# Kernel optimization log

Hardware: AMD Instinct MI355X
Metric: run time of the kernel (lower is better)

## Reference

```python
import jax, jax.numpy as jnp
import numpy as np

N = 2048          # n_nodes
H = 8             # nheads
ALPHA = 0.2       # leaky-relu slope
NEG = -9e15       # mask value used by pyGAT
# (in_dim, per-head hidden, out_dim) for the six GAT blocks of GMHAAE(256, ...)
DIMS = [(256, 128, 128), (128, 256, 256), (256, 512, 384),
        (384, 512, 256), (256, 256, 128), (128, 128, 256)]


def setup_inputs() -> dict:
    key = jax.random.key(0)
    ks = jax.random.split(key, 64)
    inp = {}
    inp["x"] = jax.random.normal(ks[0], (N, 256), dtype=jnp.float32)
    a = (jax.random.uniform(ks[1], (N, N)) < 0.01).astype(jnp.float32)
    adj = jnp.clip(jnp.maximum(a, a.T) + jnp.eye(N, dtype=jnp.float32), 0.0, 1.0)
    inp["adj"] = adj
    ki = 2
    for i, (fin, hid, fout) in enumerate(DIMS, start=1):
        s1 = (2.0 / (fin + hid)) ** 0.5
        inp[f"p{i}_Wh"] = jax.random.normal(ks[ki], (H, fin, hid), dtype=jnp.float32) * s1; ki += 1
        inp[f"p{i}_ah"] = jax.random.normal(ks[ki], (H, 2 * hid), dtype=jnp.float32) * 0.1; ki += 1
        s2 = (2.0 / (H * hid + fout)) ** 0.5
        inp[f"p{i}_Wo"] = jax.random.normal(ks[ki], (H * hid, fout), dtype=jnp.float32) * s2; ki += 1
        inp[f"p{i}_ao"] = jax.random.normal(ks[ki], (2 * fout,), dtype=jnp.float32) * 0.1; ki += 1
    return inp


def _gat_block(x, adj, Wh, ah, Wo, ao):
    """pyGAT GAT block: H concat heads (elu) -> single out head -> elu. Eval mode (no dropout)."""
    n = x.shape[0]
    D = Wh.shape[2]
    h = jnp.einsum('nf,hfd->hnd', x, Wh)                       # [H,N,D]
    s1 = jnp.einsum('hnd,hd->hn', h, ah[:, :D])                # a^T [Wh_i]
    s2 = jnp.einsum('hnd,hd->hn', h, ah[:, D:])                # a^T [Wh_j]
    e = jax.nn.leaky_relu(s1[:, :, None] + s2[:, None, :], ALPHA)   # [H,N,N]
    att = jax.nn.softmax(jnp.where(adj[None] > 0, e, NEG), axis=-1)
    hcat = jax.nn.elu(jnp.einsum('hnm,hmd->hnd', att, h))      # concat=True -> elu per head
    hcat = hcat.transpose(1, 0, 2).reshape(n, -1)              # [N, H*D]
    # output attention head (concat=False)
    D2 = Wo.shape[1]
    ho = hcat @ Wo                                             # [N,D2]
    eo = jax.nn.leaky_relu((ho @ ao[:D2])[:, None] + (ho @ ao[D2:])[None, :], ALPHA)
    ato = jax.nn.softmax(jnp.where(adj > 0, eo, NEG), axis=-1)
    return jax.nn.elu(ato @ ho)                                # F.elu in GAT.forward


def reference(x, adj,
              p1_Wh, p1_ah, p1_Wo, p1_ao,
              p2_Wh, p2_ah, p2_Wo, p2_ao,
              p3_Wh, p3_ah, p3_Wo, p3_ao,
              p4_Wh, p4_ah, p4_Wo, p4_ao,
              p5_Wh, p5_ah, p5_Wo, p5_ao,
              p6_Wh, p6_ah, p6_Wo, p6_ao):
    layers = [(p1_Wh, p1_ah, p1_Wo, p1_ao), (p2_Wh, p2_ah, p2_Wo, p2_ao),
              (p3_Wh, p3_ah, p3_Wo, p3_ao), (p4_Wh, p4_ah, p4_Wo, p4_ao),
              (p5_Wh, p5_ah, p5_Wo, p5_ao), (p6_Wh, p6_ah, p6_Wo, p6_ao)]
    h = x
    for (Wh, ah, Wo, ao) in layers:   # fixed 6-layer encoder-decoder stack
        h = _gat_block(h, adj, Wh, ah, Wo, ao)
    return h
```

## Files before the change

kernel.cpp:

```cpp
#include <hip/hip_runtime.h>
#include <hip/hip_bf16.h>
#include <math.h>

#define NN 2048
#define NH 8
#define LRALPHA 0.2f

typedef short bf16x8 __attribute__((ext_vector_type(8)));
typedef float f32x4  __attribute__((ext_vector_type(4)));

static __device__ __forceinline__ float lrelu(float x){ return x > 0.f ? x : LRALPHA * x; }
static __device__ __forceinline__ float elu(float x){ return x > 0.f ? x : expm1f(x); }

static __device__ __forceinline__ unsigned short f2bf(float v){
    unsigned u = __float_as_uint(v);
    unsigned r = (u + 0x7fffu + ((u >> 16) & 1u)) >> 16;
    return (unsigned short)r;
}
static __device__ __forceinline__ float bf2f(unsigned short b){
    return __uint_as_float(((unsigned)b) << 16);
}
static __device__ __forceinline__ float blo(unsigned u){ return __uint_as_float(u << 16); }
static __device__ __forceinline__ float bhi(unsigned u){ return __uint_as_float(u & 0xffff0000u); }

static __device__ __forceinline__ void gload16(const void* g, void* l){
    __builtin_amdgcn_global_load_lds((const __attribute__((address_space(1))) void*)g,
                                     (__attribute__((address_space(3))) void*)l, 16, 0, 0);
}

__global__ void k_count(const float* __restrict__ adj, int* __restrict__ deg) {
    int gw   = (blockIdx.x * blockDim.x + threadIdx.x) >> 6;
    int lane = threadIdx.x & 63;
    if (gw >= NN) return;
    const float* row = adj + (size_t)gw * NN;
    int cnt = 0;
    for (int j = lane; j < NN; j += 64) cnt += (row[j] > 0.f) ? 1 : 0;
    #pragma unroll
    for (int off = 32; off; off >>= 1) cnt += __shfl_down(cnt, off);
    if (lane == 0) deg[gw] = cnt;
}

__global__ void k_scan(const int* __restrict__ deg, int* __restrict__ rp) {
    __shared__ int a[NN], b[NN];
    int t = threadIdx.x;
    for (int i = t; i < NN; i += 1024) a[i] = deg[i];
    __syncthreads();
    int* src = a; int* dst = b;
    for (int off = 1; off < NN; off <<= 1) {
        for (int i = t; i < NN; i += 1024)
            dst[i] = src[i] + (i >= off ? src[i - off] : 0);
        __syncthreads();
        int* tmp = src; src = dst; dst = tmp;
    }
    for (int i = t; i < NN; i += 1024) rp[i + 1] = src[i];
    if (t == 0) rp[0] = 0;
}

__global__ void k_fill(const float* __restrict__ adj, const int* __restrict__ rp,
                       int* __restrict__ ci) {
    int gw   = (blockIdx.x * blockDim.x + threadIdx.x) >> 6;
    int lane = threadIdx.x & 63;
    if (gw >= NN) return;
    const float* row = adj + (size_t)gw * NN;
    int base = rp[gw];
    for (int j0 = 0; j0 < NN; j0 += 64) {
        bool v = row[j0 + lane] > 0.f;
        unsigned long long m = __ballot(v);
        int pos = __popcll(m & ((1ULL << lane) - 1ULL));
        if (v) ci[base + pos] = j0 + lane;
        base += __popcll(m);
    }
}

__global__ void k_split(const float* __restrict__ src, unsigned short* __restrict__ hi,
                        unsigned short* __restrict__ lo, int n4) {
    int i = blockIdx.x * 256 + threadIdx.x;
    if (i >= n4) return;
    float4 v = ((const float4*)src)[i];
    ushort4 h, l;
    h.x = f2bf(v.x); l.x = f2bf(v.x - bf2f(h.x));
    h.y = f2bf(v.y); l.y = f2bf(v.y - bf2f(h.y));
    h.z = f2bf(v.z); l.z = f2bf(v.z - bf2f(h.z));
    h.w = f2bf(v.w); l.w = f2bf(v.w - bf2f(h.w));
    ((ushort4*)hi)[i] = h;
    ((ushort4*)lo)[i] = l;
}

struct TSDesc {
    const float* B[12];
    unsigned short* bh[12];
    unsigned short* bl[12];
    int K[12], Nc[12], hs[12];
    int start[13];
};

__global__ __launch_bounds__(256) void k_tsplit_all(TSDesc d) {
    __shared__ float t[64][65];
    int b = blockIdx.x;
    int s = 0;
    while (b >= d.start[s + 1]) s++;
    int lb = b - d.start[s];
    int K = d.K[s], Nc = d.Nc[s], hs = d.hs[s];
    int tilesX = K >> 6;
    int kb = (lb % tilesX) * 64, cb = (lb / tilesX) * 64;
    const float* B = d.B[s];
    unsigned short* bth = d.bh[s];
    unsigned short* btl = d.bl[s];

    int tid = threadIdx.x;
    #pragma unroll
    for (int i = 0; i < 16; i++) {
        int idx = i * 256 + tid;
        int kk = idx >> 6, cc = idx & 63;
        int c = cb + cc, k = kb + kk;
        float v;
        if (hs < 0) v = B[(size_t)k * Nc + c];
        else {
            int hid = 1 << hs; int head = c >> hs; int dd = c & (hid - 1);
            v = B[((size_t)head * K + k) * hid + dd];
        }
        t[kk][cc] = v;
    }
    __syncthreads();
    #pragma unroll
    for (int i = 0; i < 16; i++) {
        int idx = i * 256 + tid;
        int cc = idx >> 6, kk = idx & 63;
        float v = t[kk][cc];
        unsigned short h = f2bf(v);
        size_t o = (size_t)(cb + cc) * K + kb + kk;
        bth[o] = h;
        btl[o] = f2bf(v - bf2f(h));
    }
}

template<int OUT, int NT>
__global__ __launch_bounds__(256) void k_mfma(
    const unsigned short* __restrict__ Ah, const unsigned short* __restrict__ Al,
    const unsigned short* __restrict__ Bh, const unsigned short* __restrict__ Bl,
    float* __restrict__ Cf, unsigned short* __restrict__ Cb, int Nc, int K, int Kc,
    const float* __restrict__ avec, float* __restrict__ sg1, float* __restrict__ sg2,
    int hs, int aoff, int nx, int nz, int zcol)
{
    constexpr int ALB = 4096;
    constexpr int BHB = (NT == 3) ? 8192 : 4096;
    constexpr int BLB = BHB + 2048;
    __shared__ unsigned short lds[(NT == 3) ? 12288 : 8192];
    int tid = threadIdx.x, lane = tid & 63, w = tid >> 6;

    int g = blockIdx.x;
    int xcd = g & 7, q = g >> 3;
    int x, y, z;
    if (zcol) {
        int zper = nz >> 3;
        z = xcd + 8 * (q % zper);
        int r = q / zper;
        int nxy = nx * 16;
        int r2 = r + xcd * (nxy >> 3); if (r2 >= nxy) r2 -= nxy;
        x = r2 % nx; y = r2 / nx;
    } else {
        y = xcd + 8 * (q & 1);
        x = q >> 1; z = 0;
    }
    int m0 = y * 128, n0 = x * 64;
    int kbeg = z * Kc;

    int ra0 = tid >> 2;       int ga0 = ((tid & 3) - (ra0 >> 1)) & 3;
    int ra1 = 64 + (tid >> 2); int ga1 = ((tid & 3) - (ra1 >> 1)) & 3;
    int rb  = tid >> 2;       int gb  = ((tid & 3) - (rb >> 1)) & 3;
    const unsigned short* pAh0 = Ah + (size_t)(m0 + ra0) * K + kbeg + ga0 * 8;
    const unsigned short* pAh1 = Ah + (size_t)(m0 + ra1) * K + kbeg + ga1 * 8;
    const unsigned short* pAl0 = (NT == 3) ? Al + (size_t)(m0 + ra0) * K + kbeg + ga0 * 8 : nullptr;
    const unsigned short* pAl1 = (NT == 3) ? Al + (size_t)(m0 + ra1) * K + kbeg + ga1 * 8 : nullptr;
    const unsigned short* pBh  = Bh + (size_t)(n0 + rb) * K + kbeg + gb * 8;
    const unsigned short* pBl  = Bl + (size_t)(n0 + rb) * K + kbeg + gb * 8;
    unsigned short* dA0 = &lds[w * 512];
    unsigned short* dA1 = &lds[2048 + w * 512];
    unsigned short* dB  = &lds[BHB + w * 512];

    int wr = w >> 1, wc = w & 1;
    int offA[4], offB[2];
    #pragma unroll
    for (int m = 0; m < 4; m++) {
        int row = wr * 64 + m * 16 + (lane & 15); int gg = lane >> 4;
        offA[m] = (row * 4 + ((gg + (row >> 1)) & 3)) * 8;
    }
    #pragma unroll
    for (int n = 0; n < 2; n++) {
        int row = wc * 32 + n * 16 + (lane & 15); int gg = lane >> 4;
        offB[n] = (row * 4 + ((gg + (row >> 1)) & 3)) * 8;
    }

    f32x4 acc[4][2];
    #pragma unroll
    for (int m = 0; m < 4; m++)
        #pragma unroll
        for (int n = 0; n < 2; n++) acc[m][n] = (f32x4){0.f, 0.f, 0.f, 0.f};

    int nk = Kc >> 5;
    for (int ks = 0; ks < nk; ks++) {
        gload16(pAh0, dA0);
        gload16(pAh1, dA1);
        if (NT == 3) { gload16(pAl0, dA0 + ALB); gload16(pAl1, dA1 + ALB); }
        gload16(pBh, dB);
        gload16(pBl, dB + 2048);
        pAh0 += 32; pAh1 += 32;
        if (NT == 3) { pAl0 += 32; pAl1 += 32; }
        pBh += 32; pBl += 32;
        __syncthreads();
        bf16x8 ah[4], al[4], bh[2], bl[2];
        #pragma unroll
        for (int m = 0; m < 4; m++) {
            ah[m] = *(const bf16x8*)&lds[offA[m]];
            if (NT == 3) al[m] = *(const bf16x8*)&lds[ALB + offA[m]];
        }
        #pragma unroll
        for (int n = 0; n < 2; n++) {
            bh[n] = *(const bf16x8*)&lds[BHB + offB[n]];
            bl[n] = *(const bf16x8*)&lds[BLB + offB[n]];
        }
        #pragma unroll
        for (int m = 0; m < 4; m++)
            #pragma unroll
            for (int n = 0; n < 2; n++) {
                acc[m][n] = __builtin_amdgcn_mfma_f32_16x16x32_bf16(ah[m], bh[n], acc[m][n], 0, 0, 0);
                if (NT == 3)
                    acc[m][n] = __builtin_amdgcn_mfma_f32_16x16x32_bf16(al[m], bh[n], acc[m][n], 0, 0, 0);
                acc[m][n] = __builtin_amdgcn_mfma_f32_16x16x32_bf16(ah[m], bl[n], acc[m][n], 0, 0, 0);
            }
        __syncthreads();
    }

    #pragma unroll
    for (int m = 0; m < 4; m++)
        #pragma unroll
        for (int n = 0; n < 2; n++) {
            int row = m0 + wr * 64 + m * 16 + (lane >> 4) * 4;
            int col = n0 + wc * 32 + n * 16 + (lane & 15);
            #pragma unroll
            for (int r = 0; r < 4; r++) {
                float v = acc[m][n][r];
                if (OUT == 0) Cb[(size_t)(row + r) * Nc + col] = f2bf(v);
                else          atomicAdd(&Cf[(size_t)(row + r) * Nc + col], v);
            }
        }

    int head = (hs >= 0) ? (n0 >> hs) : 0;
    const float* ab = avec + head * 2 * aoff;
    float av1[2], av2[2];
    int colbase = n0 + wc * 32 + (lane & 15);
    #pragma unroll
    for (int n = 0; n < 2; n++) {
        int c = colbase + n * 16;
        int dd = (hs >= 0) ? (c & (aoff - 1)) : c;
        av1[n] = ab[dd];
        av2[n] = ab[dd + aoff];
    }
    #pragma unroll
    for (int m = 0; m < 4; m++)
        #pragma unroll
        for (int r = 0; r < 4; r++) {
            float p1 = 0.f, p2 = 0.f;
            #pragma unroll
            for (int n = 0; n < 2; n++) {
                float v = acc[m][n][r];
                p1 += v * av1[n];
                p2 += v * av2[n];
            }
            #pragma unroll
            for (int o = 1; o < 16; o <<= 1) {
                p1 += __shfl_xor(p1, o);
                p2 += __shfl_xor(p2, o);
            }
            if ((lane & 15) == 0) {
                int row = m0 + wr * 64 + m * 16 + (lane >> 4) * 4 + r;
                atomicAdd(&sg1[head * NN + row], p1);
                atomicAdd(&sg2[head * NN + row], p2);
            }
        }
}

__global__ __launch_bounds__(64) void k_aggb(
    const unsigned short* __restrict__ hh, const float* __restrict__ s1,
    const float* __restrict__ s2, const int* __restrict__ rp, const int* __restrict__ ci,
    unsigned short* __restrict__ outH, int hid, int HD, int c8sh)
{
    __shared__ float    wls[64];
    __shared__ unsigned cls[64];

    int blk  = blockIdx.x;
    int head = blk & (NH - 1);
    int i    = blk >> 3;
    int lane = threadIdx.x;
    int base = rp[i], deg = rp[i + 1] - base;
    float s1i = s1[head * NN + i];
    const float* s2h = s2 + head * NN;

    int C8  = 1 << c8sh;
    int G   = 64 >> c8sh;
    int col = lane & (C8 - 1);
    int grp = lane >> c8sh;

    const uint4* h4 = (const uint4*)hh;
    unsigned hoff8 = (unsigned)(head * hid) >> 3;
    unsigned ld8   = (unsigned)HD >> 3;

    float m_run = -1e30f, s_run = 0.f;
    float a0=0,a1=0,a2=0,a3=0,a4=0,a5=0,a6=0,a7=0;

    for (int k0 = 0; k0 < deg; k0 += 64) {
        int n = min(64, deg - k0);
        float e = -1e30f;
        unsigned coff = 0;
        if (lane < n) {
            int j = ci[base + k0 + lane];
            e = lrelu(s1i + s2h[j]);
            coff = (unsigned)j * ld8 + hoff8;
        }
        float bm = e;
        #pragma unroll
        for (int o = 32; o; o >>= 1) bm = fmaxf(bm, __shfl_xor(bm, o));
        float m2 = fmaxf(m_run, bm);
        float wv = (lane < n) ? expf(e - m2) : 0.f;
        float bs = wv;
        #pragma unroll
        for (int o = 32; o; o >>= 1) bs += __shfl_xor(bs, o);
        float scale = expf(m_run - m2);
        s_run = s_run * scale + bs;
        a0*=scale; a1*=scale; a2*=scale; a3*=scale;
        a4*=scale; a5*=scale; a6*=scale; a7*=scale;
        m_run = m2;
        wls[lane] = wv;
        cls[lane] = coff;

        float q0=0,q1=0,q2=0,q3=0,q4=0,q5=0,q6=0,q7=0;
        int k = grp;
        for (; k + G < n; k += 2 * G) {
            float w0 = wls[k], w1 = wls[k + G];
            uint4 u0 = h4[cls[k]     + col];
            uint4 u1 = h4[cls[k + G] + col];
            a0 += w0 * blo(u0.x); a1 += w0 * bhi(u0.x);
            a2 += w0 * blo(u0.y); a3 += w0 * bhi(u0.y);
            a4 += w0 * blo(u0.z); a5 += w0 * bhi(u0.z);
            a6 += w0 * blo(u0.w); a7 += w0 * bhi(u0.w);
            q0 += w1 * blo(u1.x); q1 += w1 * bhi(u1.x);
            q2 += w1 * blo(u1.y); q3 += w1 * bhi(u1.y);
            q4 += w1 * blo(u1.z); q5 += w1 * bhi(u1.z);
            q6 += w1 * blo(u1.w); q7 += w1 * bhi(u1.w);
        }
        if (k < n) {
            float w0 = wls[k];
            uint4 u0 = h4[cls[k] + col];
            a0 += w0 * blo(u0.x); a1 += w0 * bhi(u0.x);
            a2 += w0 * blo(u0.y); a3 += w0 * bhi(u0.y);
            a4 += w0 * blo(u0.z); a5 += w0 * bhi(u0.z);
            a6 += w0 * blo(u0.w); a7 += w0 * bhi(u0.w);
        }
        a0+=q0; a1+=q1; a2+=q2; a3+=q3; a4+=q4; a5+=q5; a6+=q6; a7+=q7;
    }

    #pragma unroll
    for (int o = 64; o > 1; o >>= 1) {
        if (o > C8) {
            int m = o >> 1;
            a0 += __shfl_xor(a0, m); a1 += __shfl_xor(a1, m);
            a2 += __shfl_xor(a2, m); a3 += __shfl_xor(a3, m);
            a4 += __shfl_xor(a4, m); a5 += __shfl_xor(a5, m);
            a6 += __shfl_xor(a6, m); a7 += __shfl_xor(a7, m);
        }
    }

    if (grp == 0) {
        float inv = 1.f / s_run;
        float v[8] = {a0*inv,a1*inv,a2*inv,a3*inv,a4*inv,a5*inv,a6*inv,a7*inv};
        #pragma unroll
        for (int e2 = 0; e2 < 8; e2++) v[e2] = elu(v[e2]);
        unsigned short hh_[8];
        #pragma unroll
        for (int e2 = 0; e2 < 8; e2++) hh_[e2] = f2bf(v[e2]);
        size_t ob = ((size_t)i * HD + head * hid) >> 3;
        uint4 ph;
        ph.x = (unsigned)hh_[0] | ((unsigned)hh_[1] << 16);
        ph.y = (unsigned)hh_[2] | ((unsigned)hh_[3] << 16);
        ph.z = (unsigned)hh_[4] | ((unsigned)hh_[5] << 16);
        ph.w = (unsigned)hh_[6] | ((unsigned)hh_[7] << 16);
        ((uint4*)outH)[ob + col] = ph;
    }
}

__global__ __launch_bounds__(64) void k_aggs(
    const float* __restrict__ hsrc, const float* __restrict__ t1, const float* __restrict__ t2,
    const int* __restrict__ rp, const int* __restrict__ ci,
    float* __restrict__ outF, unsigned short* __restrict__ outH,
    int fout, int SCtot)
{
    __shared__ float    wls[64];
    __shared__ unsigned cls[64];

    int blk = blockIdx.x;
    int i   = blk / SCtot;
    int sc  = blk - i * SCtot;
    int lane = threadIdx.x;
    int base = rp[i], deg = rp[i + 1] - base;
    float s1i = t1[i];

    int C4tot = fout >> 2;
    int soff  = sc * 64;
    int C4s   = min(64, C4tot - soff);
    int c4sh  = 31 - __clz(C4s);
    int col = lane & (C4s - 1);
    int grp = lane >> c4sh;
    int G   = 64 >> c4sh;

    const float4* h4 = (const float4*)hsrc;
    unsigned ld4 = (unsigned)fout >> 2;

    float m_run = -1e30f, s_run = 0.f;
    float4 acc = make_float4(0.f, 0.f, 0.f, 0.f);

    for (int k0 = 0; k0 < deg; k0 += 64) {
        int n = min(64, deg - k0);
        float e = -1e30f;
        unsigned coff = 0;
        if (lane < n) {
            int j = ci[base + k0 + lane];
            e = lrelu(s1i + t2[j]);
            coff = (unsigned)j * ld4 + soff;
        }
        float bm = e;
        #pragma unroll
        for (int o = 32; o; o >>= 1) bm = fmaxf(bm, __shfl_xor(bm, o));
        float m2 = fmaxf(m_run, bm);
        float wv = (lane < n) ? expf(e - m2) : 0.f;
        float bs = wv;
        #pragma unroll
        for (int o = 32; o; o >>= 1) bs += __shfl_xor(bs, o);
        float scale = expf(m_run - m2);
        s_run = s_run * scale + bs;
        acc.x *= scale; acc.y *= scale; acc.z *= scale; acc.w *= scale;
        m_run = m2;
        wls[lane] = wv;
        cls[lane] = coff;

        float4 q = make_float4(0,0,0,0);
        int k = grp;
        for (; k + G < n; k += 2 * G) {
            float w0 = wls[k], w1 = wls[k + G];
            float4 h0 = h4[cls[k]     + col];
            float4 h1 = h4[cls[k + G] + col];
            acc.x += w0 * h0.x; acc.y += w0 * h0.y; acc.z += w0 * h0.z; acc.w += w0 * h0.w;
            q.x   += w1 * h1.x; q.y   += w1 * h1.y; q.z   += w1 * h1.z; q.w   += w1 * h1.w;
        }
        if (k < n) {
            float w0 = wls[k];
            float4 h0 = h4[cls[k] + col];
            acc.x += w0 * h0.x; acc.y += w0 * h0.y; acc.z += w0 * h0.z; acc.w += w0 * h0.w;
        }
        acc.x += q.x; acc.y += q.y; acc.z += q.z; acc.w += q.w;
    }

    #pragma unroll
    for (int o = 64; o > 1; o >>= 1) {
        if (o > C4s) {
            int m = o >> 1;
            acc.x += __shfl_xor(acc.x, m); acc.y += __shfl_xor(acc.y, m);
            acc.z += __shfl_xor(acc.z, m); acc.w += __shfl_xor(acc.w, m);
        }
    }

    if (grp == 0) {
        float inv = 1.f / s_run;
        float4 val;
        val.x = elu(acc.x * inv); val.y = elu(acc.y * inv);
        val.z = elu(acc.z * inv); val.w = elu(acc.w * inv);
        size_t o4 = (size_t)i * ld4 + soff + col;
        if (outF) ((float4*)outF)[o4] = val;
        ushort4 h;
        h.x = f2bf(val.x); h.y = f2bf(val.y);
        h.z = f2bf(val.z); h.w = f2bf(val.w);
        ((ushort4*)outH)[o4] = h;
    }
}

extern "C" void kernel_launch(void* const* d_in, const int* in_sizes, int n_in,
                              void* d_out, int out_size, void* d_ws, size_t ws_size,
                              hipStream_t stream)
{
    const float* x   = (const float*)d_in[0];
    const float* adj = (const float*)d_in[1];
    struct L { int fin, hid, fout; };
    const L dims[6] = {{256,128,128},{128,256,256},{256,512,384},
                       {384,512,256},{256,256,128},{128,128,256}};
    const int SKwo[6] = {16, 8, 8, 8, 16, 8};
    const int SB = 2 * NH * NN + 2 * NN;

    char* ws = (char*)d_ws;
    size_t off = 0;
    auto alloc = [&](size_t bytes) -> void* {
        void* p = ws + off;
        off = (off + bytes + 255) & ~(size_t)255;
        return p;
    };
    int*   rp   = (int*)alloc((NN + 1) * sizeof(int));
    int*   deg  = (int*)alloc(NN * sizeof(int));
    int*   ci   = (int*)alloc((size_t)(1 << 20) * sizeof(int));
    unsigned short* hh  = (unsigned short*)alloc((size_t)NN * 4096 * 2);
    unsigned short* ghi = (unsigned short*)alloc((size_t)NN * 4096 * 2);
    unsigned short* xhi = (unsigned short*)alloc((size_t)NN * 512 * 2);
    unsigned short* xlo = (unsigned short*)alloc((size_t)NN * 512 * 2);
    float* sball  = (float*)alloc((size_t)6 * SB * sizeof(float));
    float* hoball = (float*)alloc((size_t)NN * 1408 * sizeof(float));

    int hoboff[6]; { int acc = 0; for (int l = 0; l < 6; l++) { hoboff[l] = acc; acc += dims[l].fout; } }

    unsigned short* whh[6]; unsigned short* whl[6];
    unsigned short* woh[6]; unsigned short* wol[6];
    TSDesc td;
    int nblk = 0;
    for (int l = 0; l < 6; l++) {
        int fin = dims[l].fin, hid = dims[l].hid, fout = dims[l].fout;
        int HD = NH * hid;
        size_t szWh = (size_t)fin * HD, szWo = (size_t)HD * fout;
        whh[l] = (unsigned short*)alloc(szWh * 2);
        whl[l] = (unsigned short*)alloc(szWh * 2);
        woh[l] = (unsigned short*)alloc(szWo * 2);
        wol[l] = (unsigned short*)alloc(szWo * 2);
        int hs = (hid == 128) ? 7 : (hid == 256) ? 8 : 9;
        td.B[2*l] = (const float*)d_in[2 + l * 4 + 0];
        td.bh[2*l] = whh[l]; td.bl[2*l] = whl[l];
        td.K[2*l] = fin; td.Nc[2*l] = HD; td.hs[2*l] = hs;
        td.start[2*l] = nblk; nblk += (fin / 64) * (HD / 64);
        td.B[2*l+1] = (const float*)d_in[2 + l * 4 + 2];
        td.bh[2*l+1] = woh[l]; td.bl[2*l+1] = wol[l];
        td.K[2*l+1] = HD; td.Nc[2*l+1] = fout; td.hs[2*l+1] = -1;
        td.start[2*l+1] = nblk; nblk += (HD / 64) * (fout / 64);
    }
    td.start[12] = nblk;

    hipMemsetAsync(sball, 0, (size_t)6 * SB * sizeof(float), stream);
    hipMemsetAsync(hoball, 0, (size_t)NN * 1408 * sizeof(float), stream);
    k_count<<<NN / 4, 256, 0, stream>>>(adj, deg);
    k_scan <<<1, 1024, 0, stream>>>(deg, rp);
    k_fill <<<NN / 4, 256, 0, stream>>>(adj, rp, ci);
    k_split<<<(NN * 256 / 4 + 255) / 256, 256, 0, stream>>>(x, xhi, xlo, NN * 256 / 4);
    k_tsplit_all<<<nblk, 256, 0, stream>>>(td);

    for (int l = 0; l < 6; l++) {
        int fin = dims[l].fin, hid = dims[l].hid, fout = dims[l].fout;
        int HD = NH * hid;
        int hs = (hid == 128) ? 7 : (hid == 256) ? 8 : 9;
        int c8sh = hs - 3;
        const float* ah = (const float*)d_in[2 + l * 4 + 1];
        const float* ao = (const float*)d_in[2 + l * 4 + 3];

        float* s1 = sball + (size_t)l * SB;
        float* s2 = s1 + NH * NN;
        float* t1 = s2 + NH * NN;
        float* t2 = t1 + NN;
        float* hob = hoball + (size_t)NN * hoboff[l];

        int nx1 = HD / 64;
        if (l == 0)
            k_mfma<0,3><<<nx1 * 16, 256, 0, stream>>>(xhi, xlo, whh[l], whl[l], nullptr, hh, HD,
                                                      fin, fin, ah, s1, s2, hs, hid, nx1, 1, 0);
        else
            k_mfma<0,2><<<nx1 * 16, 256, 0, stream>>>(xhi, nullptr, whh[l], whl[l], nullptr, hh, HD,
                                                      fin, fin, ah, s1, s2, hs, hid, nx1, 1, 0);

        k_aggb<<<NN * NH, 64, 0, stream>>>(hh, s1, s2, rp, ci, ghi, hid, HD, c8sh);

        int sko = SKwo[l];
        int nx2 = fout / 64;
        k_mfma<1,2><<<nx2 * 16 * sko, 256, 0, stream>>>(ghi, nullptr, woh[l], wol[l], hob, nullptr,
                                                        fout, HD, HD / sko, ao, t1, t2, -1, fout,
                                                        nx2, sko, 1);

        float* outF = (l == 5) ? (float*)d_out : nullptr;
        int SCtot = (fout / 4 + 63) / 64;
        k_aggs<<<NN * SCtot, 64, 0, stream>>>(hob, t1, t2, rp, ci, outF, xhi, fout, SCtot);
    }
}
```

Measured before the change: 534.0 us.

## Replace split-K atomic accumulation with partial buffers and a reduction kernel

The split-K output-projection GEMM now stores each K-slice's fp32 tile in its own slice of a partial buffer instead of atomically adding into a zeroed accumulator, and it no longer computes the attention score dots itself. A new per-row kernel sums the slices, writes the projected features and computes the two output-attention score vectors in one pass. This drops the large memset and the global float atomics for the feature tile and the score vectors, and makes the result deterministic. In exchange it writes and re-reads several full copies of the output, up to 16 for some layers, and adds one kernel launch per layer.

```diff
diff --git a/kernel.cpp b/kernel.cpp
--- a/kernel.cpp
+++ b/kernel.cpp
@@ -231,6 +231,7 @@
         __syncthreads();
     }
 
+    size_t pbase = (size_t)z * NN * Nc;
     #pragma unroll
     for (int m = 0; m < 4; m++)
         #pragma unroll
@@ -241,43 +242,75 @@
             for (int r = 0; r < 4; r++) {
                 float v = acc[m][n][r];
                 if (OUT == 0) Cb[(size_t)(row + r) * Nc + col] = f2bf(v);
-                else          atomicAdd(&Cf[(size_t)(row + r) * Nc + col], v);
+                else          Cf[pbase + (size_t)(row + r) * Nc + col] = v;
             }
         }
 
-    int head = (hs >= 0) ? (n0 >> hs) : 0;
-    const float* ab = avec + head * 2 * aoff;
-    float av1[2], av2[2];
-    int colbase = n0 + wc * 32 + (lane & 15);
-    #pragma unroll
-    for (int n = 0; n < 2; n++) {
-        int c = colbase + n * 16;
-        int dd = (hs >= 0) ? (c & (aoff - 1)) : c;
-        av1[n] = ab[dd];
-        av2[n] = ab[dd + aoff];
-    }
-    #pragma unroll
-    for (int m = 0; m < 4; m++)
-        #pragma unroll
-        for (int r = 0; r < 4; r++) {
-            float p1 = 0.f, p2 = 0.f;
+    if (OUT == 0) {
+        int head = (hs >= 0) ? (n0 >> hs) : 0;
+        const float* ab = avec + head * 2 * aoff;
+        float av1[2], av2[2];
+        int colbase = n0 + wc * 32 + (lane & 15);
+        #pragma unroll
+        for (int n = 0; n < 2; n++) {
+            int c = colbase + n * 16;
+            int dd = (hs >= 0) ? (c & (aoff - 1)) : c;
+            av1[n] = ab[dd];
+            av2[n] = ab[dd + aoff];
+        }
+        #pragma unroll
+        for (int m = 0; m < 4; m++)
             #pragma unroll
-            for (int n = 0; n < 2; n++) {
-                float v = acc[m][n][r];
-                p1 += v * av1[n];
-                p2 += v * av2[n];
+            for (int r = 0; r < 4; r++) {
+                float p1 = 0.f, p2 = 0.f;
+                #pragma unroll
+                for (int n = 0; n < 2; n++) {
+                    float v = acc[m][n][r];
+                    p1 += v * av1[n];
+                    p2 += v * av2[n];
+                }
+                #pragma unroll
+                for (int o = 1; o < 16; o <<= 1) {
+                    p1 += __shfl_xor(p1, o);
+                    p2 += __shfl_xor(p2, o);
+                }
+                if ((lane & 15) == 0) {
+                    int row = m0 + wr * 64 + m * 16 + (lane >> 4) * 4 + r;
+                    atomicAdd(&sg1[head * NN + row], p1);
+                    atomicAdd(&sg2[head * NN + row], p2);
+                }
             }
-            #pragma unroll
-            for (int o = 1; o < 16; o <<= 1) {
-                p1 += __shfl_xor(p1, o);
-                p2 += __shfl_xor(p2, o);
-            }
-            if ((lane & 15) == 0) {
-                int row = m0 + wr * 64 + m * 16 + (lane >> 4) * 4 + r;
-                atomicAdd(&sg1[head * NN + row], p1);
-                atomicAdd(&sg2[head * NN + row], p2);
-            }
-        }
+    }
+}
+
+__global__ __launch_bounds__(64) void k_red(
+    const float* __restrict__ part, float* __restrict__ ho,
+    const float* __restrict__ ao, float* __restrict__ t1, float* __restrict__ t2,
+    int fout, int sko)
+{
+    int row = blockIdx.x;
+    int lane = threadIdx.x;
+    int C4 = fout >> 2;
+    const float4* p4 = (const float4*)part;
+    size_t stride4 = (size_t)NN * C4;
+    float d1 = 0.f, d2 = 0.f;
+    for (int c = lane; c < C4; c += 64) {
+        size_t o = (size_t)row * C4 + c;
+        float4 s = p4[o];
+        for (int zz = 1; zz < sko; zz++) {
+            float4 v = p4[o + (size_t)zz * stride4];
+            s.x += v.x; s.y += v.y; s.z += v.z; s.w += v.w;
+        }
+        ((float4*)ho)[o] = s;
+        int cc = c * 4;
+        d1 += s.x * ao[cc]        + s.y * ao[cc + 1]
+            + s.z * ao[cc + 2]    + s.w * ao[cc + 3];
+        d2 += s.x * ao[fout + cc]     + s.y * ao[fout + cc + 1]
+            + s.z * ao[fout + cc + 2] + s.w * ao[fout + cc + 3];
+    }
+    #pragma unroll
+    for (int o = 32; o; o >>= 1) { d1 += __shfl_xor(d1, o); d2 += __shfl_xor(d2, o); }
+    if (lane == 0) { t1[row] = d1; t2[row] = d2; }
 }
 
 __global__ __launch_bounds__(64) void k_aggb(
@@ -492,7 +525,7 @@
     const L dims[6] = {{256,128,128},{128,256,256},{256,512,384},
                        {384,512,256},{256,256,128},{128,128,256}};
     const int SKwo[6] = {16, 8, 8, 8, 16, 8};
-    const int SB = 2 * NH * NN + 2 * NN;
+    const int SB = 2 * NH * NN;
 
     char* ws = (char*)d_ws;
     size_t off = 0;
@@ -509,9 +542,9 @@
     unsigned short* xhi = (unsigned short*)alloc((size_t)NN * 512 * 2);
     unsigned short* xlo = (unsigned short*)alloc((size_t)NN * 512 * 2);
     float* sball  = (float*)alloc((size_t)6 * SB * sizeof(float));
-    float* hoball = (float*)alloc((size_t)NN * 1408 * sizeof(float));
-
-    int hoboff[6]; { int acc = 0; for (int l = 0; l < 6; l++) { hoboff[l] = acc; acc += dims[l].fout; } }
+    float* hopart = (float*)alloc((size_t)NN * 3072 * sizeof(float));
+    float* ho     = (float*)alloc((size_t)NN * 384 * sizeof(float));
+    float* t12    = (float*)alloc((size_t)2 * NN * sizeof(float));
 
     unsigned short* whh[6]; unsigned short* whl[6];
     unsigned short* woh[6]; unsigned short* wol[6];
@@ -538,7 +571,6 @@
     td.start[12] = nblk;
 
     hipMemsetAsync(sball, 0, (size_t)6 * SB * sizeof(float), stream);
-    hipMemsetAsync(hoball, 0, (size_t)NN * 1408 * sizeof(float), stream);
     k_count<<<NN / 4, 256, 0, stream>>>(adj, deg);
     k_scan <<<1, 1024, 0, stream>>>(deg, rp);
     k_fill <<<NN / 4, 256, 0, stream>>>(adj, rp, ci);
@@ -555,9 +587,8 @@
 
         float* s1 = sball + (size_t)l * SB;
         float* s2 = s1 + NH * NN;
-        float* t1 = s2 + NH * NN;
-        float* t2 = t1 + NN;
-        float* hob = hoball + (size_t)NN * hoboff[l];
+        float* t1 = t12;
+        float* t2 = t12 + NN;
 
         int nx1 = HD / 64;
         if (l == 0)
@@ -571,12 +602,15 @@
 
         int sko = SKwo[l];
         int nx2 = fout / 64;
-        k_mfma<1,2><<<nx2 * 16 * sko, 256, 0, stream>>>(ghi, nullptr, woh[l], wol[l], hob, nullptr,
-                                                        fout, HD, HD / sko, ao, t1, t2, -1, fout,
+        k_mfma<1,2><<<nx2 * 16 * sko, 256, 0, stream>>>(ghi, nullptr, woh[l], wol[l], hopart,
+                                                        nullptr, fout, HD, HD / sko,
+                                                        nullptr, nullptr, nullptr, -1, fout,
                                                         nx2, sko, 1);
+
+        k_red<<<NN, 64, 0, stream>>>(hopart, ho, ao, t1, t2, fout, sko);
 
         float* outF = (l == 5) ? (float*)d_out : nullptr;
         int SCtot = (fout / 4 + 63) / 64;
-        k_aggs<<<NN * SCtot, 64, 0, stream>>>(hob, t1, t2, rp, ci, outF, xhi, fout, SCtot);
-    }
-}
+        k_aggs<<<NN * SCtot, 64, 0, stream>>>(ho, t1, t2, rp, ci, outF, xhi, fout, SCtot);
+    }
+}
```

Measured after the change: 449.6 us. -15.8%, faster.
